# Kernel tuning notes

Measured on AMD Instinct MI355X. Metric: run time of the kernel, lower is better.

The kernel has to match this reference:

```python
import jax, jax.numpy as jnp
import numpy as np

B, N, IN, HID, H, OUT = 32, 512, 64, 64, 4, 64
NEG_SLOPE = 0.2
NEG_INF = -1e9


def setup_inputs() -> dict:
    key = jax.random.key(0)
    ks = jax.random.split(key, 10)
    s = 0.1
    return {
        "x": jax.random.normal(ks[0], (B, N, IN), jnp.float32),
        "adj": jax.random.randint(ks[1], (B, N, N), 0, 2, jnp.int32),
        "W1": jax.random.normal(ks[2], (IN, H * HID), jnp.float32) * s,
        "a1_src": jax.random.normal(ks[3], (H, HID), jnp.float32) * s,
        "a1_dst": jax.random.normal(ks[4], (H, HID), jnp.float32) * s,
        "b1": jnp.zeros((H * HID,), jnp.float32),
        "W2": jax.random.normal(ks[5], (H * HID, OUT), jnp.float32) * s,
        "a2_src": jax.random.normal(ks[6], (1, OUT), jnp.float32) * s,
        "a2_dst": jax.random.normal(ks[7], (1, OUT), jnp.float32) * s,
        "b2": jnp.zeros((OUT,), jnp.float32),
    }


def _gat_layer(x, mask, W, a_src, a_dst, b, heads, feat):
    # x: [N, Fin]; mask: [N_dst, N_src] bool (edge src->dst), self-loops included
    h = (x @ W).reshape(N, heads, feat)              # [N, H, F]
    e_src = jnp.einsum('nhf,hf->nh', h, a_src)       # [N, H]
    e_dst = jnp.einsum('nhf,hf->nh', h, a_dst)       # [N, H]
    # scores[d, s, h] = leaky_relu(a_dst.x_d + a_src.x_s)
    scores = jax.nn.leaky_relu(e_dst[:, None, :] + e_src[None, :, :], NEG_SLOPE)
    scores = jnp.where(mask[:, :, None], scores, NEG_INF)
    alpha = jax.nn.softmax(scores, axis=1)           # segment-softmax over src neighbors
    out = jnp.einsum('dsh,shf->dhf', alpha, h)       # aggregate messages
    return out.reshape(N, heads * feat) + b


def reference(x, adj, W1, a1_src, a1_dst, b1, W2, a2_src, a2_dst, b2):
    eye = jnp.eye(N, dtype=bool)

    def one_graph(xi, ai):
        # edge i->j when adj[i, j] != 0 (coo row=src, col=dst); add self-loops
        mask = (ai != 0).T | eye                     # [dst, src]
        h1 = jax.nn.elu(_gat_layer(xi, mask, W1, a1_src, a1_dst, b1, H, HID))
        return _gat_layer(h1, mask, W2, a2_src, a2_dst, b2, 1, OUT)

    return jax.vmap(one_graph)(x, adj)               # [B, N, OUT]
```

## Files before the change

kernel.cpp:

```cpp
#include <hip/hip_runtime.h>
#include <cstddef>

#define NN 512
#define NEG_SLOPE 0.2f

typedef __attribute__((ext_vector_type(8))) short short8;
typedef __attribute__((ext_vector_type(16))) float f32x16;

__device__ __forceinline__ unsigned short f2bf(float v) {
  unsigned u = __float_as_uint(v);
  return (unsigned short)((u + 0x7FFFu + ((u >> 16) & 1u)) >> 16);
}

__global__ __launch_bounds__(256) void k_g1m(const int* __restrict__ adj,
                                             const float* __restrict__ x,
                                             const float* __restrict__ W1,
                                             const float* __restrict__ a1s,
                                             const float* __restrict__ a1d,
                                             unsigned* __restrict__ mask,
                                             unsigned short* __restrict__ hb1,
                                             float* __restrict__ e1s,
                                             float* __restrict__ e1d) {
  __shared__ float tile[32 * 36];
  int i = blockIdx.x;
  int b = (i & 7) * 4 + ((i >> 3) & 3), mt = i >> 5;
  int d0 = mt * 32;
  int t = threadIdx.x;

  if (t >= 64) {
    int t2 = t - 64;
    const int* abase = adj + (size_t)b * NN * NN;
    for (int u = t2; u < 512; u += 192) {
      int d = d0 + (u & 31), w = u >> 5;
      unsigned wv = 0;
#pragma unroll
      for (int j = 0; j < 32; ++j) {
        int s = w * 32 + j;
        unsigned bit = ((abase[(size_t)s * NN + d] != 0) || (s == d)) ? 1u : 0u;
        wv |= bit << j;
      }
      mask[((size_t)b * 16 + w) * NN + d] = wv;
    }
    return;
  }

  int lane = t, m = lane & 31, kg = lane >> 5;
  const float* xrow = x + ((size_t)b * NN + d0 + m) * 64 + kg * 8;
  short8 a[4];
#pragma unroll
  for (int kt = 0; kt < 4; ++kt) {
    float4 v0 = *(const float4*)(xrow + kt * 16);
    float4 v1 = *(const float4*)(xrow + kt * 16 + 4);
    short8 r;
    r[0] = (short)f2bf(v0.x); r[1] = (short)f2bf(v0.y);
    r[2] = (short)f2bf(v0.z); r[3] = (short)f2bf(v0.w);
    r[4] = (short)f2bf(v1.x); r[5] = (short)f2bf(v1.y);
    r[6] = (short)f2bf(v1.z); r[7] = (short)f2bf(v1.w);
    a[kt] = r;
  }
  short8* hb8 = (short8*)hb1;
  short8 wf[2][4];
#pragma unroll
  for (int kt = 0; kt < 4; ++kt) {
    int k0 = kt * 16 + kg * 8;
    short8 r;
#pragma unroll
    for (int j = 0; j < 8; ++j) r[j] = (short)f2bf(W1[(k0 + j) * 256 + m]);
    wf[0][kt] = r;
  }
  float e_h = 0.f;
#pragma unroll
  for (int nt = 0; nt < 8; ++nt) {
    int cur = nt & 1;
    if (nt < 7) {
      int f = (nt + 1) * 32 + m;
#pragma unroll
      for (int kt = 0; kt < 4; ++kt) {
        int k0 = kt * 16 + kg * 8;
        short8 r;
#pragma unroll
        for (int j = 0; j < 8; ++j) r[j] = (short)f2bf(W1[(k0 + j) * 256 + f]);
        wf[cur ^ 1][kt] = r;
      }
    }
    f32x16 acc;
#pragma unroll
    for (int q = 0; q < 16; ++q) acc[q] = 0.f;
#pragma unroll
    for (int kt = 0; kt < 4; ++kt)
      acc = __builtin_amdgcn_mfma_f32_32x32x16_bf16(a[kt], wf[cur][kt], acc, 0, 0, 0);
#pragma unroll
    for (int reg = 0; reg < 16; ++reg) {
      int row = (reg & 3) + 8 * (reg >> 2) + 4 * kg;
      tile[row * 36 + m] = acc[reg];
    }
    int h = nt >> 1, ft = nt & 1;
#pragma unroll
    for (int ktl = 0; ktl < 2; ++ktl) {
      short8 r;
#pragma unroll
      for (int j = 0; j < 8; ++j)
        r[j] = (short)f2bf(tile[(ktl * 16 + kg * 8 + j) * 36 + m]);
      hb8[((((size_t)b * 4 + h) * 32 + mt * 2 + ktl) * 2 + ft) * 64 + lane] = r;
    }
    const float* coeff = (kg ? a1d : a1s) + h * 64 + ft * 32;
    float ep = 0.f;
#pragma unroll
    for (int c4 = 0; c4 < 8; ++c4) {
      float4 tv = *(const float4*)&tile[m * 36 + c4 * 4];
      float4 cv = *(const float4*)&coeff[c4 * 4];
      ep += tv.x * cv.x + tv.y * cv.y + tv.z * cv.z + tv.w * cv.w;
    }
    e_h += ep;
    if (ft) {
      float* p = kg ? e1d : e1s;
      p[((size_t)b * 4 + h) * NN + d0 + m] = e_h;
      e_h = 0.f;
    }
  }
}

__global__ __launch_bounds__(256) void k_attn1g2(const unsigned* __restrict__ mask,
                                                 const unsigned short* __restrict__ hb1,
                                                 const float* __restrict__ e1s,
                                                 const float* __restrict__ e1d,
                                                 const float* __restrict__ b1,
                                                 const float* __restrict__ W2,
                                                 const float* __restrict__ a2s,
                                                 const float* __restrict__ a2d,
                                                 unsigned short* __restrict__ hb2,
                                                 float* __restrict__ e2s,
                                                 float* __restrict__ e2d) {
  __shared__ float es[4 * NN];
  __shared__ unsigned mw[16 * 32];
  __shared__ unsigned short ht[32 * 264];
  __shared__ float tile2[2][32 * 36];
  int i = blockIdx.x;
  int b = (i & 7) * 4 + ((i >> 3) & 3), mt = i >> 5;
  int d0 = mt * 32;
  int t = threadIdx.x;
  const float* esrc = e1s + (size_t)b * 4 * NN;
#pragma unroll
  for (int q = 0; q < 8; ++q) es[t + q * 256] = esrc[t + q * 256];
  const unsigned* msrc = mask + (size_t)b * 16 * NN + d0;
  mw[t] = msrc[(t >> 5) * NN + (t & 31)];
  {
    int idx = t + 256;
    mw[idx] = msrc[(idx >> 5) * NN + (idx & 31)];
  }
  __syncthreads();
  int h = t >> 6, lane = t & 63, m = lane & 31, kg = lane >> 5;
  float ed = e1d[((size_t)b * 4 + h) * NN + d0 + m];
  const short8* bfr = (const short8*)hb1 + ((size_t)b * 4 + h) * 32 * 2 * 64;
  f32x16 acc0, acc1;
#pragma unroll
  for (int q = 0; q < 16; ++q) { acc0[q] = 0.f; acc1[q] = 0.f; }
  float l = 0.f;
  for (int kt = 0; kt < 32; ++kt) {
    unsigned wv = mw[(kt >> 1) * 32 + m];
    int shift = (kt & 1) * 16 + kg * 8;
    const float* ep = &es[h * NN + kt * 16 + kg * 8];
    short8 a;
#pragma unroll
    for (int j = 0; j < 8; ++j) {
      float sc = ed + ep[j];
      sc = fmaxf(sc, NEG_SLOPE * sc);
      float pv = __expf(sc);
      pv = ((wv >> (shift + j)) & 1u) ? pv : 0.f;
      l += pv;
      a[j] = (short)f2bf(pv);
    }
    short8 bv0 = bfr[(kt * 2 + 0) * 64 + lane];
    short8 bv1 = bfr[(kt * 2 + 1) * 64 + lane];
    acc0 = __builtin_amdgcn_mfma_f32_32x32x16_bf16(a, bv0, acc0, 0, 0, 0);
    acc1 = __builtin_amdgcn_mfma_f32_32x32x16_bf16(a, bv1, acc1, 0, 0, 0);
  }
  float lf = l + __shfl(l, lane ^ 32, 64);
  float linv = 1.f / lf;
  float bia0 = b1[h * 64 + m];
  float bia1 = b1[h * 64 + 32 + m];
#pragma unroll
  for (int reg = 0; reg < 16; ++reg) {
    int row = (reg & 3) + 8 * (reg >> 2) + 4 * kg;
    float li = __shfl(linv, row, 64);
    float v0 = acc0[reg] * li + bia0;
    v0 = (v0 > 0.f) ? v0 : (__expf(v0) - 1.f);
    float v1 = acc1[reg] * li + bia1;
    v1 = (v1 > 0.f) ? v1 : (__expf(v1) - 1.f);
    ht[row * 264 + h * 64 + m] = f2bf(v0);
    ht[row * 264 + h * 64 + 32 + m] = f2bf(v1);
  }
  __syncthreads();
  int w2 = t >> 6;
  if (w2 < 2) {
    int nt = w2;
    short8 wfr[16];
#pragma unroll
    for (int kt = 0; kt < 16; ++kt) {
      int k0 = kt * 16 + kg * 8;
      short8 r;
#pragma unroll
      for (int j = 0; j < 8; ++j)
        r[j] = (short)f2bf(W2[(k0 + j) * 64 + nt * 32 + m]);
      wfr[kt] = r;
    }
    f32x16 acc;
#pragma unroll
    for (int q = 0; q < 16; ++q) acc[q] = 0.f;
#pragma unroll
    for (int kt = 0; kt < 16; ++kt) {
      short8 av = *(const short8*)&ht[m * 264 + kt * 16 + kg * 8];
      acc = __builtin_amdgcn_mfma_f32_32x32x16_bf16(av, wfr[kt], acc, 0, 0, 0);
    }
    float* tw = tile2[nt];
#pragma unroll
    for (int reg = 0; reg < 16; ++reg) {
      int row = (reg & 3) + 8 * (reg >> 2) + 4 * kg;
      tw[row * 36 + m] = acc[reg];
    }
  }
  __syncthreads();
  if (w2 < 2) {
    const float* tw = tile2[w2];
    short8* hb8 = (short8*)hb2;
#pragma unroll
    for (int ktl = 0; ktl < 2; ++ktl) {
      short8 r;
#pragma unroll
      for (int j = 0; j < 8; ++j)
        r[j] = (short)f2bf(tw[(ktl * 16 + kg * 8 + j) * 36 + m]);
      hb8[(((size_t)b * 32 + mt * 2 + ktl) * 2 + w2) * 64 + lane] = r;
    }
  } else {
    const float* coeff = ((w2 == 2) ? a2s : a2d) + kg * 32;
    const float* tsrc = tile2[kg];
    float val = 0.f;
#pragma unroll
    for (int c4 = 0; c4 < 8; ++c4) {
      float4 tv = *(const float4*)&tsrc[m * 36 + c4 * 4];
      float4 cv = *(const float4*)&coeff[c4 * 4];
      val += tv.x * cv.x + tv.y * cv.y + tv.z * cv.z + tv.w * cv.w;
    }
    float tot = val + __shfl(val, lane ^ 32, 64);
    if (kg == 0) {
      float* p = (w2 == 2) ? e2s : e2d;
      p[(size_t)b * NN + d0 + m] = tot;
    }
  }
}

__global__ __launch_bounds__(256) void k_attn2(const unsigned* __restrict__ mask,
                                               const unsigned short* __restrict__ hb2,
                                               const float* __restrict__ e2s,
                                               const float* __restrict__ e2d,
                                               const float* __restrict__ b2,
                                               float* __restrict__ out) {
  __shared__ float es[NN];
  __shared__ unsigned mw[16 * 32];
  __shared__ float cred[4][2][16][64];
  __shared__ float lred[4][64];
  __shared__ float linv_s[32];
  int i = blockIdx.x;
  int b = (i & 7) * 4 + ((i >> 3) & 3);
  int d0 = (i >> 5) * 32;
  int t = threadIdx.x;
  es[t] = e2s[(size_t)b * NN + t];
  es[t + 256] = e2s[(size_t)b * NN + t + 256];
  const unsigned* msrc = mask + (size_t)b * 16 * NN + d0;
  mw[t] = msrc[(t >> 5) * NN + (t & 31)];
  {
    int idx = t + 256;
    mw[idx] = msrc[(idx >> 5) * NN + (idx & 31)];
  }
  __syncthreads();
  int w = t >> 6, lane = t & 63, m = lane & 31, kg = lane >> 5;
  float ed = e2d[(size_t)b * NN + d0 + m];
  const short8* bfr = (const short8*)hb2 + (size_t)b * 32 * 2 * 64;
  f32x16 acc0, acc1;
#pragma unroll
  for (int q = 0; q < 16; ++q) { acc0[q] = 0.f; acc1[q] = 0.f; }
  float l = 0.f;
#pragma unroll
  for (int kk = 0; kk < 8; ++kk) {
    int kt = w * 8 + kk;
    unsigned wv = mw[(kt >> 1) * 32 + m];
    int shift = (kt & 1) * 16 + kg * 8;
    const float* ep = &es[kt * 16 + kg * 8];
    short8 a;
#pragma unroll
    for (int j = 0; j < 8; ++j) {
      float sc = ed + ep[j];
      sc = fmaxf(sc, NEG_SLOPE * sc);
      float pv = __expf(sc);
      pv = ((wv >> (shift + j)) & 1u) ? pv : 0.f;
      l += pv;
      a[j] = (short)f2bf(pv);
    }
    short8 bv0 = bfr[(kt * 2 + 0) * 64 + lane];
    short8 bv1 = bfr[(kt * 2 + 1) * 64 + lane];
    acc0 = __builtin_amdgcn_mfma_f32_32x32x16_bf16(a, bv0, acc0, 0, 0, 0);
    acc1 = __builtin_amdgcn_mfma_f32_32x32x16_bf16(a, bv1, acc1, 0, 0, 0);
  }
  lred[w][lane] = l;
#pragma unroll
  for (int reg = 0; reg < 16; ++reg) {
    cred[w][0][reg][lane] = acc0[reg];
    cred[w][1][reg][lane] = acc1[reg];
  }
  __syncthreads();
  if (t < 32) {
    float s = 0.f;
#pragma unroll
    for (int q = 0; q < 4; ++q) s += lred[q][t] + lred[q][t + 32];
    linv_s[t] = 1.f / s;
  }
  __syncthreads();
#pragma unroll
  for (int q = 0; q < 8; ++q) {
    int pos = t + q * 256;
    int nt = pos >> 10;
    int rem = pos & 1023;
    int reg = rem >> 6;
    int ln = rem & 63;
    float v = cred[0][nt][reg][ln] + cred[1][nt][reg][ln] +
              cred[2][nt][reg][ln] + cred[3][nt][reg][ln];
    int row = (reg & 3) + 8 * (reg >> 2) + 4 * (ln >> 5);
    int col = nt * 32 + (ln & 31);
    out[((size_t)b * NN + d0 + row) * 64 + col] = v * linv_s[row] + b2[col];
  }
}

extern "C" void kernel_launch(void* const* d_in, const int* in_sizes, int n_in,
                              void* d_out, int out_size, void* d_ws, size_t ws_size,
                              hipStream_t stream) {
  const float* x = (const float*)d_in[0];
  const int* adj = (const int*)d_in[1];
  const float* W1 = (const float*)d_in[2];
  const float* a1s = (const float*)d_in[3];
  const float* a1d = (const float*)d_in[4];
  const float* b1 = (const float*)d_in[5];
  const float* W2 = (const float*)d_in[6];
  const float* a2s = (const float*)d_in[7];
  const float* a2d = (const float*)d_in[8];
  const float* b2 = (const float*)d_in[9];
  float* out = (float*)d_out;

  char* w = (char*)d_ws;
  unsigned* mask = (unsigned*)w;
  unsigned short* hb1 = (unsigned short*)(w + (4u << 20));
  float* e1s = (float*)(w + (12u << 20));
  float* e1d = (float*)(w + (12u << 20) + (256u << 10));
  unsigned short* hb2 = (unsigned short*)(w + (21u << 20));
  float* e2s = (float*)(w + (23u << 20));
  float* e2d = (float*)(w + (23u << 20) + (64u << 10));

  hipLaunchKernelGGL(k_g1m, dim3(512), dim3(256), 0, stream, adj, x, W1, a1s,
                     a1d, mask, hb1, e1s, e1d);
  hipLaunchKernelGGL(k_attn1g2, dim3(512), dim3(256), 0, stream, mask, hb1,
                     e1s, e1d, b1, W2, a2s, a2d, hb2, e2s, e2d);
  hipLaunchKernelGGL(k_attn2, dim3(512), dim3(256), 0, stream, mask, hb2, e2s,
                     e2d, b2, out);
}
```

Before: 140.3 us.

## Stage W1 as bf16 in LDS and pre-pack W2 MFMA fragments once

In k_g1m, each block now loads all of W1 with coalesced float4 reads, converts it to bf16 and stores it in shared memory. The MFMA B fragments are then read from LDS instead of through strided global gathers with per-element conversion. The first 16 blocks also pre-pack W2 into bf16 short8 fragment order in workspace, so k_attn1g2 loads each fragment as a single vector instead of gathering and converting 8 scalars. The cost is about 33 KB of extra LDS per k_g1m block, which may reduce occupancy, plus a redundant full W1 load and convert in every block and a rearranged workspace layout.

```diff
diff --git a/kernel.cpp b/kernel.cpp
--- a/kernel.cpp
+++ b/kernel.cpp
@@ -15,23 +15,51 @@
 __global__ __launch_bounds__(256) void k_g1m(const int* __restrict__ adj,
                                              const float* __restrict__ x,
                                              const float* __restrict__ W1,
+                                             const float* __restrict__ W2,
                                              const float* __restrict__ a1s,
                                              const float* __restrict__ a1d,
                                              unsigned* __restrict__ mask,
                                              unsigned short* __restrict__ hb1,
                                              float* __restrict__ e1s,
-                                             float* __restrict__ e1d) {
+                                             float* __restrict__ e1d,
+                                             short8* __restrict__ W2B) {
+  __shared__ __align__(16) unsigned short w1p[64 * 260];
   __shared__ float tile[32 * 36];
   int i = blockIdx.x;
   int b = (i & 7) * 4 + ((i >> 3) & 3), mt = i >> 5;
   int d0 = mt * 32;
   int t = threadIdx.x;
 
+  const float4* w4 = (const float4*)W1;
+#pragma unroll
+  for (int r = 0; r < 16; ++r) {
+    int idx = t + r * 256;
+    float4 v = w4[idx];
+    int k = idx >> 6;
+    int f0 = (idx & 63) * 4;
+    unsigned lo = (unsigned)f2bf(v.x) | ((unsigned)f2bf(v.y) << 16);
+    unsigned hi = (unsigned)f2bf(v.z) | ((unsigned)f2bf(v.w) << 16);
+    *(uint2*)&w1p[k * 260 + f0] = make_uint2(lo, hi);
+  }
+  __syncthreads();
+
   if (t >= 64) {
+    if (i < 16 && t < 192) {
+      int fi = i * 128 + (t - 64);
+      int unit = fi >> 6, lane = fi & 63;
+      int nt = unit >> 4, kt = unit & 15;
+      int f = nt * 32 + (lane & 31);
+      int k0 = kt * 16 + ((lane >> 5) << 3);
+      short8 r;
+#pragma unroll
+      for (int j = 0; j < 8; ++j) r[j] = (short)f2bf(W2[(k0 + j) * 64 + f]);
+      W2B[fi] = r;
+    }
     int t2 = t - 64;
     const int* abase = adj + (size_t)b * NN * NN;
     for (int u = t2; u < 512; u += 192) {
-      int d = d0 + (u & 31), w = u >> 5;
+      int dl = u & 31, w = u >> 5;
+      int d = d0 + dl;
       unsigned wv = 0;
 #pragma unroll
       for (int j = 0; j < 32; ++j) {
@@ -59,36 +87,24 @@
     a[kt] = r;
   }
   short8* hb8 = (short8*)hb1;
-  short8 wf[2][4];
-#pragma unroll
-  for (int kt = 0; kt < 4; ++kt) {
-    int k0 = kt * 16 + kg * 8;
-    short8 r;
-#pragma unroll
-    for (int j = 0; j < 8; ++j) r[j] = (short)f2bf(W1[(k0 + j) * 256 + m]);
-    wf[0][kt] = r;
-  }
   float e_h = 0.f;
 #pragma unroll
   for (int nt = 0; nt < 8; ++nt) {
-    int cur = nt & 1;
-    if (nt < 7) {
-      int f = (nt + 1) * 32 + m;
-#pragma unroll
-      for (int kt = 0; kt < 4; ++kt) {
-        int k0 = kt * 16 + kg * 8;
-        short8 r;
-#pragma unroll
-        for (int j = 0; j < 8; ++j) r[j] = (short)f2bf(W1[(k0 + j) * 256 + f]);
-        wf[cur ^ 1][kt] = r;
-      }
+    short8 wfr[4];
+#pragma unroll
+    for (int kt = 0; kt < 4; ++kt) {
+      int base = (kt * 16 + kg * 8) * 260 + nt * 32 + m;
+      short8 r;
+#pragma unroll
+      for (int j = 0; j < 8; ++j) r[j] = (short)w1p[base + j * 260];
+      wfr[kt] = r;
     }
     f32x16 acc;
 #pragma unroll
     for (int q = 0; q < 16; ++q) acc[q] = 0.f;
 #pragma unroll
     for (int kt = 0; kt < 4; ++kt)
-      acc = __builtin_amdgcn_mfma_f32_32x32x16_bf16(a[kt], wf[cur][kt], acc, 0, 0, 0);
+      acc = __builtin_amdgcn_mfma_f32_32x32x16_bf16(a[kt], wfr[kt], acc, 0, 0, 0);
 #pragma unroll
     for (int reg = 0; reg < 16; ++reg) {
       int row = (reg & 3) + 8 * (reg >> 2) + 4 * kg;
@@ -125,7 +141,7 @@
                                                  const float* __restrict__ e1s,
                                                  const float* __restrict__ e1d,
                                                  const float* __restrict__ b1,
-                                                 const float* __restrict__ W2,
+                                                 const short8* __restrict__ W2B,
                                                  const float* __restrict__ a2s,
                                                  const float* __restrict__ a2d,
                                                  unsigned short* __restrict__ hb2,
@@ -196,14 +212,7 @@
     int nt = w2;
     short8 wfr[16];
 #pragma unroll
-    for (int kt = 0; kt < 16; ++kt) {
-      int k0 = kt * 16 + kg * 8;
-      short8 r;
-#pragma unroll
-      for (int j = 0; j < 8; ++j)
-        r[j] = (short)f2bf(W2[(k0 + j) * 64 + nt * 32 + m]);
-      wfr[kt] = r;
-    }
+    for (int kt = 0; kt < 16; ++kt) wfr[kt] = W2B[(nt * 16 + kt) * 64 + lane];
     f32x16 acc;
 #pragma unroll
     for (int q = 0; q < 16; ++q) acc[q] = 0.f;
@@ -346,18 +355,19 @@
   float* out = (float*)d_out;
 
   char* w = (char*)d_ws;
-  unsigned* mask = (unsigned*)w;
-  unsigned short* hb1 = (unsigned short*)(w + (4u << 20));
+  short8* W2B = (short8*)w;
+  unsigned* mask = (unsigned*)(w + (128u << 10));
+  unsigned short* hb1 = (unsigned short*)(w + (2u << 20));
   float* e1s = (float*)(w + (12u << 20));
   float* e1d = (float*)(w + (12u << 20) + (256u << 10));
-  unsigned short* hb2 = (unsigned short*)(w + (21u << 20));
-  float* e2s = (float*)(w + (23u << 20));
-  float* e2d = (float*)(w + (23u << 20) + (64u << 10));
-
-  hipLaunchKernelGGL(k_g1m, dim3(512), dim3(256), 0, stream, adj, x, W1, a1s,
-                     a1d, mask, hb1, e1s, e1d);
+  unsigned short* hb2 = (unsigned short*)(w + (16u << 20));
+  float* e2s = (float*)(w + (20u << 20));
+  float* e2d = (float*)(w + (20u << 20) + (64u << 10));
+
+  hipLaunchKernelGGL(k_g1m, dim3(512), dim3(256), 0, stream, adj, x, W1, W2,
+                     a1s, a1d, mask, hb1, e1s, e1d, W2B);
   hipLaunchKernelGGL(k_attn1g2, dim3(512), dim3(256), 0, stream, mask, hb1,
-                     e1s, e1d, b1, W2, a2s, a2d, hb2, e2s, e2d);
+                     e1s, e1d, b1, W2B, a2s, a2d, hb2, e2s, e2d);
   hipLaunchKernelGGL(k_attn2, dim3(512), dim3(256), 0, stream, mask, hb2, e2s,
                      e2d, b2, out);
 }
```

Result: faster. 126.1 us (-10.1%).
